# Kernel tuning notes

Measured on AMD Instinct MI355X. Metric: run time of the kernel, lower is better.

Reference implementation:

```python
import jax, jax.numpy as jnp
import numpy as np

QMIN, QMAX = -128.0, 127.0  # symmetric int8 (bit_width=8)

def setup_inputs() -> dict:
    key = jax.random.key(0)
    k1, k2, k3, k4, k5 = jax.random.split(key, 5)
    x = jax.random.normal(k1, (16, 4096, 1024), dtype=jnp.float32)
    weight_int = jax.random.randint(k2, (1024, 1024), 0, 127, dtype=jnp.int32)
    bias_int = jax.random.randint(k3, (1024,), 0, 127, dtype=jnp.int32)
    input_scale = jax.random.uniform(k4, (), dtype=jnp.float32, minval=0.01, maxval=1.0)
    output_scale = jax.random.uniform(k5, (), dtype=jnp.float32, minval=0.01, maxval=1.0)
    return {
        "x": x,
        "weight_int": weight_int,
        "bias_int": bias_int,
        "input_scale": input_scale,
        "output_scale": output_scale,
        "input_zero_point": 0,
        "output_zero_point": 0,
    }

def reference(x, weight_int, bias_int, input_scale, output_scale,
              input_zero_point, output_zero_point):
    # quantize input: round(x/scale)+zp, clamp to int8 range (kept in fp32,
    # matching x_int.float() in the original before the GEMM)
    x_q = jnp.clip(jnp.round(x / input_scale) + input_zero_point, QMIN, QMAX)
    # F.linear(x_q, W, b): [B,S,K] @ [N,K]^T + [N]
    out_int = jnp.einsum('bsk,nk->bsn', x_q, weight_int.astype(jnp.float32))
    out_int = out_int + bias_int.astype(jnp.float32)
    # dequantize output
    return (out_int - output_zero_point) * output_scale
```

## Files before the change

kernel.cpp:

```cpp
#include <hip/hip_runtime.h>
#include <stdint.h>

typedef int v4i __attribute__((ext_vector_type(4)));

#define AS1(p) ((const __attribute__((address_space(1))) void*)(p))
#define AS3(p) ((__attribute__((address_space(3))) void*)(p))

__global__ __launch_bounds__(256) void quant_x_kernel(
    const float* __restrict__ x, int8_t* __restrict__ xq,
    const float* __restrict__ s_p, const int* __restrict__ izp_p, int n16)
{
    int t = blockIdx.x * 256 + threadIdx.x;
    if (t >= n16) return;
    float s = *s_p;
    float zp = (float)(*izp_p);
    const float4* xin = (const float4*)x + (size_t)t * 4;
    int words[4];
#pragma unroll
    for (int i = 0; i < 4; ++i) {
        float4 v = xin[i];
        float q0 = fminf(127.f, fmaxf(-128.f, rintf(v.x / s) + zp));
        float q1 = fminf(127.f, fmaxf(-128.f, rintf(v.y / s) + zp));
        float q2 = fminf(127.f, fmaxf(-128.f, rintf(v.z / s) + zp));
        float q3 = fminf(127.f, fmaxf(-128.f, rintf(v.w / s) + zp));
        words[i] = ((int)q0 & 255) | (((int)q1 & 255) << 8) |
                   (((int)q2 & 255) << 16) | (((int)q3 & 255) << 24);
    }
    ((int4*)xq)[t] = make_int4(words[0], words[1], words[2], words[3]);
}

__global__ __launch_bounds__(256) void pack_w_kernel(
    const int* __restrict__ w, int8_t* __restrict__ w8, int n4)
{
    int t = blockIdx.x * 256 + threadIdx.x;
    if (t >= n4) return;
    int4 v = ((const int4*)w)[t];
    ((int*)w8)[t] = (v.x & 255) | ((v.y & 255) << 8) |
                    ((v.z & 255) << 16) | ((v.w & 255) << 24);
}

#define GM 65536
#define GN 1024
#define GK 1024
#define NT 8

__global__ __launch_bounds__(512, 2) void gemm_i8_kernel(
    const int8_t* __restrict__ A,
    const int8_t* __restrict__ B,
    const int* __restrict__ bias,
    const float* __restrict__ osc_p, const int* __restrict__ ozp_p,
    float* __restrict__ out)
{
    __shared__ int8_t As[2][32768];
    __shared__ int8_t Bs[2][32768];

    const int tid = threadIdx.x;
    const int w   = tid >> 6, l = tid & 63;
    const int wm  = w >> 2,  wn = w & 3;
    const int r15 = l & 15,  s4 = l >> 4;

    const int wg = blockIdx.x;
    const int lg = ((wg & 7) << 7) + (wg >> 3);
    const int bm0 = (lg >> 2) << 8;
    const int bn0 = (lg & 3) << 8;

    const int srow = tid >> 3;
    const int gcol = (((tid & 7) ^ ((tid >> 3) & 7)) << 4);
    const int8_t* aS = A + (size_t)(bm0 + srow) * GK + gcol;
    const int8_t* bS = B + (size_t)(bn0 + srow) * GK + gcol;

#define SHOT_A(T, BUF, C) __builtin_amdgcn_global_load_lds( \
    AS1(aS + (size_t)(C) * 64 * GK + (T) * 128), \
    AS3(&As[BUF][(C) * 8192 + w * 1024]), 16, 0, 0)
#define SHOT_B(T, BUF, C) __builtin_amdgcn_global_load_lds( \
    AS1(bS + (size_t)(C) * 64 * GK + (T) * 128), \
    AS3(&Bs[BUF][(C) * 8192 + w * 1024]), 16, 0, 0)

    const int akey = r15 & 7;
    const int a_rd0 = ((wm * 128 + r15) << 7) + (((0 + s4) ^ akey) << 4);
    const int a_rd1 = ((wm * 128 + r15) << 7) + (((4 + s4) ^ akey) << 4);
    const int b_rd0 = ((wn * 64 + r15) << 7) + (((0 + s4) ^ akey) << 4);
    const int b_rd1 = ((wn * 64 + r15) << 7) + (((4 + s4) ^ akey) << 4);

    v4i acc[8][4];
#pragma unroll
    for (int i = 0; i < 8; ++i)
#pragma unroll
        for (int j = 0; j < 4; ++j) acc[i][j] = (v4i){0, 0, 0, 0};

    v4i bfr[4][2];

#define LOADB(CUR) do { \
    _Pragma("unroll") \
    for (int j = 0; j < 4; ++j) { \
        bfr[j][0] = *(const v4i*)&Bs[CUR][b_rd0 + j * 2048]; \
        bfr[j][1] = *(const v4i*)&Bs[CUR][b_rd1 + j * 2048]; \
    } \
} while (0)

#define PHASE(CUR, Q, ...) do { \
    v4i af0 = *(const v4i*)&As[CUR][a_rd0 + (Q) * 4096]; \
    v4i af1 = *(const v4i*)&As[CUR][a_rd1 + (Q) * 4096]; \
    v4i af2 = *(const v4i*)&As[CUR][a_rd0 + (Q) * 4096 + 2048]; \
    v4i af3 = *(const v4i*)&As[CUR][a_rd1 + (Q) * 4096 + 2048]; \
    __VA_ARGS__; \
    __builtin_amdgcn_s_barrier(); \
    __builtin_amdgcn_s_setprio(1); \
    _Pragma("unroll") \
    for (int j = 0; j < 4; ++j) { \
        acc[(Q)*2][j]     = __builtin_amdgcn_mfma_i32_16x16x64_i8(af0, bfr[j][0], acc[(Q)*2][j], 0, 0, 0); \
        acc[(Q)*2][j]     = __builtin_amdgcn_mfma_i32_16x16x64_i8(af1, bfr[j][1], acc[(Q)*2][j], 0, 0, 0); \
        acc[(Q)*2 + 1][j] = __builtin_amdgcn_mfma_i32_16x16x64_i8(af2, bfr[j][0], acc[(Q)*2 + 1][j], 0, 0, 0); \
        acc[(Q)*2 + 1][j] = __builtin_amdgcn_mfma_i32_16x16x64_i8(af3, bfr[j][1], acc[(Q)*2 + 1][j], 0, 0, 0); \
    } \
    __builtin_amdgcn_s_setprio(0); \
    __builtin_amdgcn_s_barrier(); \
} while (0)

#define BODY(T, SON) do { \
    const int cur_ = (T) & 1, nxt_ = cur_ ^ 1; \
    if (SON) { \
        SHOT_A((T) + 1, nxt_, 0); SHOT_A((T) + 1, nxt_, 1); \
        asm volatile("s_waitcnt vmcnt(2)" ::: "memory"); \
    } else { \
        asm volatile("s_waitcnt vmcnt(0)" ::: "memory"); \
    } \
    __builtin_amdgcn_s_barrier(); \
    __builtin_amdgcn_sched_barrier(0); \
    LOADB(cur_); \
    PHASE(cur_, 0, if (SON) { SHOT_A((T) + 1, nxt_, 2); SHOT_A((T) + 1, nxt_, 3); }); \
    PHASE(cur_, 1, if (SON) { SHOT_B((T) + 1, nxt_, 0); SHOT_B((T) + 1, nxt_, 1); }); \
    PHASE(cur_, 2, if (SON) { SHOT_B((T) + 1, nxt_, 2); SHOT_B((T) + 1, nxt_, 3); }); \
    PHASE(cur_, 3, ); \
} while (0)

#pragma unroll
    for (int c = 0; c < 4; ++c) { SHOT_A(0, 0, c); SHOT_B(0, 0, c); }

#pragma unroll 1
    for (int t = 0; t < NT - 1; ++t) BODY(t, 1);
    BODY(NT - 1, 0);

#undef BODY
#undef PHASE
#undef LOADB
#undef SHOT_A
#undef SHOT_B

    const float osc = *osc_p;
    const int   ozp = *ozp_p;
    int bj[4];
#pragma unroll
    for (int j = 0; j < 4; ++j)
        bj[j] = bias[bn0 + wn * 64 + j * 16 + r15] - ozp;

#pragma unroll
    for (int i = 0; i < 8; ++i) {
        const int mrow = bm0 + wm * 128 + i * 16 + s4 * 4;
#pragma unroll
        for (int j = 0; j < 4; ++j) {
            const int n = bn0 + wn * 64 + j * 16 + r15;
            float* op = out + (size_t)mrow * GN + n;
#pragma unroll
            for (int r = 0; r < 4; ++r)
                __builtin_nontemporal_store((float)(acc[i][j][r] + bj[j]) * osc,
                                            op + (size_t)r * GN);
        }
    }
}

extern "C" void kernel_launch(void* const* d_in, const int* in_sizes, int n_in,
                              void* d_out, int out_size, void* d_ws, size_t ws_size,
                              hipStream_t stream)
{
    const float* x         = (const float*)d_in[0];
    const int*   w_int     = (const int*)d_in[1];
    const int*   b_int     = (const int*)d_in[2];
    const float* in_scale  = (const float*)d_in[3];
    const float* out_scale = (const float*)d_in[4];
    const int*   izp       = (const int*)d_in[5];
    const int*   ozp       = (const int*)d_in[6];
    float* out = (float*)d_out;

    int8_t* xq = (int8_t*)d_ws;
    int8_t* w8 = (int8_t*)d_ws + (size_t)64 * 1024 * 1024;

    quant_x_kernel<<<16384, 256, 0, stream>>>(x, xq, in_scale, izp, 4194304);
    pack_w_kernel<<<1024, 256, 0, stream>>>(w_int, w8, 262144);
    gemm_i8_kernel<<<1024, 512, 0, stream>>>(xq, w8, b_int, out_scale, ozp, out);
}
```

Before: 171.3 us.

## Halve GEMM K-tile to 64 with 16 stages and fuse prep kernels

The int8 GEMM now uses a K-tile of 64 bytes instead of 128, running 16 pipeline iterations. This halves LDS use to 64 KB per block, with a new 4-way XOR swizzle and a restructured load/MFMA phase schedule. The x-quantize and weight-pack kernels are merged into one launch to save a kernel launch. The smaller tile means twice as many barriers per K and less MFMA work per sync, traded for lower LDS footprint and possibly better occupancy.

```diff
diff --git a/kernel.cpp b/kernel.cpp
--- a/kernel.cpp
+++ b/kernel.cpp
@@ -6,12 +6,20 @@
 #define AS1(p) ((const __attribute__((address_space(1))) void*)(p))
 #define AS3(p) ((__attribute__((address_space(3))) void*)(p))
 
-__global__ __launch_bounds__(256) void quant_x_kernel(
+__global__ __launch_bounds__(256) void prep_kernel(
     const float* __restrict__ x, int8_t* __restrict__ xq,
-    const float* __restrict__ s_p, const int* __restrict__ izp_p, int n16)
+    const int* __restrict__ w, int8_t* __restrict__ w8,
+    const float* __restrict__ s_p, const int* __restrict__ izp_p)
 {
-    int t = blockIdx.x * 256 + threadIdx.x;
-    if (t >= n16) return;
+    const int b = blockIdx.x;
+    if (b >= 16384) {
+        int t = (b - 16384) * 256 + threadIdx.x;
+        int4 v = ((const int4*)w)[t];
+        ((int*)w8)[t] = (v.x & 255) | ((v.y & 255) << 8) |
+                        ((v.z & 255) << 16) | ((v.w & 255) << 24);
+        return;
+    }
+    int t = b * 256 + threadIdx.x;
     float s = *s_p;
     float zp = (float)(*izp_p);
     const float4* xin = (const float4*)x + (size_t)t * 4;
@@ -29,20 +37,10 @@
     ((int4*)xq)[t] = make_int4(words[0], words[1], words[2], words[3]);
 }
 
-__global__ __launch_bounds__(256) void pack_w_kernel(
-    const int* __restrict__ w, int8_t* __restrict__ w8, int n4)
-{
-    int t = blockIdx.x * 256 + threadIdx.x;
-    if (t >= n4) return;
-    int4 v = ((const int4*)w)[t];
-    ((int*)w8)[t] = (v.x & 255) | ((v.y & 255) << 8) |
-                    ((v.z & 255) << 16) | ((v.w & 255) << 24);
-}
-
 #define GM 65536
 #define GN 1024
 #define GK 1024
-#define NT 8
+#define NT 16
 
 __global__ __launch_bounds__(512, 2) void gemm_i8_kernel(
     const int8_t* __restrict__ A,
@@ -51,8 +49,8 @@
     const float* __restrict__ osc_p, const int* __restrict__ ozp_p,
     float* __restrict__ out)
 {
-    __shared__ int8_t As[2][32768];
-    __shared__ int8_t Bs[2][32768];
+    __shared__ int8_t As[2][16384];
+    __shared__ int8_t Bs[2][16384];
 
     const int tid = threadIdx.x;
     const int w   = tid >> 6, l = tid & 63;
@@ -64,23 +62,21 @@
     const int bm0 = (lg >> 2) << 8;
     const int bn0 = (lg & 3) << 8;
 
-    const int srow = tid >> 3;
-    const int gcol = (((tid & 7) ^ ((tid >> 3) & 7)) << 4);
+    const int srow = tid >> 2;
+    const int gcol = (((tid & 3) ^ ((tid >> 3) & 3)) << 4);
     const int8_t* aS = A + (size_t)(bm0 + srow) * GK + gcol;
     const int8_t* bS = B + (size_t)(bn0 + srow) * GK + gcol;
 
 #define SHOT_A(T, BUF, C) __builtin_amdgcn_global_load_lds( \
-    AS1(aS + (size_t)(C) * 64 * GK + (T) * 128), \
+    AS1(aS + (size_t)(C) * 128 * GK + (T) * 64), \
     AS3(&As[BUF][(C) * 8192 + w * 1024]), 16, 0, 0)
 #define SHOT_B(T, BUF, C) __builtin_amdgcn_global_load_lds( \
-    AS1(bS + (size_t)(C) * 64 * GK + (T) * 128), \
+    AS1(bS + (size_t)(C) * 128 * GK + (T) * 64), \
     AS3(&Bs[BUF][(C) * 8192 + w * 1024]), 16, 0, 0)
 
-    const int akey = r15 & 7;
-    const int a_rd0 = ((wm * 128 + r15) << 7) + (((0 + s4) ^ akey) << 4);
-    const int a_rd1 = ((wm * 128 + r15) << 7) + (((4 + s4) ^ akey) << 4);
-    const int b_rd0 = ((wn * 64 + r15) << 7) + (((0 + s4) ^ akey) << 4);
-    const int b_rd1 = ((wn * 64 + r15) << 7) + (((4 + s4) ^ akey) << 4);
+    const int key = (r15 >> 1) & 3;
+    const int a_rd = ((wm * 128 + r15) << 6) + ((s4 ^ key) << 4);
+    const int b_rd = ((wn *  64 + r15) << 6) + ((s4 ^ key) << 4);
 
     v4i acc[8][4];
 #pragma unroll
@@ -88,30 +84,19 @@
 #pragma unroll
         for (int j = 0; j < 4; ++j) acc[i][j] = (v4i){0, 0, 0, 0};
 
-    v4i bfr[4][2];
+    v4i bfr[4];
 
-#define LOADB(CUR) do { \
-    _Pragma("unroll") \
-    for (int j = 0; j < 4; ++j) { \
-        bfr[j][0] = *(const v4i*)&Bs[CUR][b_rd0 + j * 2048]; \
-        bfr[j][1] = *(const v4i*)&Bs[CUR][b_rd1 + j * 2048]; \
-    } \
-} while (0)
-
-#define PHASE(CUR, Q, ...) do { \
-    v4i af0 = *(const v4i*)&As[CUR][a_rd0 + (Q) * 4096]; \
-    v4i af1 = *(const v4i*)&As[CUR][a_rd1 + (Q) * 4096]; \
-    v4i af2 = *(const v4i*)&As[CUR][a_rd0 + (Q) * 4096 + 2048]; \
-    v4i af3 = *(const v4i*)&As[CUR][a_rd1 + (Q) * 4096 + 2048]; \
-    __VA_ARGS__; \
+#define PHASE(CUR, P, STMT) do { \
+    v4i af0 = *(const v4i*)&As[CUR][a_rd + (P) * 2048]; \
+    v4i af1 = *(const v4i*)&As[CUR][a_rd + (P) * 2048 + 1024]; \
+    STMT; \
     __builtin_amdgcn_s_barrier(); \
+    asm volatile("s_waitcnt lgkmcnt(0)" ::: "memory"); \
     __builtin_amdgcn_s_setprio(1); \
     _Pragma("unroll") \
     for (int j = 0; j < 4; ++j) { \
-        acc[(Q)*2][j]     = __builtin_amdgcn_mfma_i32_16x16x64_i8(af0, bfr[j][0], acc[(Q)*2][j], 0, 0, 0); \
-        acc[(Q)*2][j]     = __builtin_amdgcn_mfma_i32_16x16x64_i8(af1, bfr[j][1], acc[(Q)*2][j], 0, 0, 0); \
-        acc[(Q)*2 + 1][j] = __builtin_amdgcn_mfma_i32_16x16x64_i8(af2, bfr[j][0], acc[(Q)*2 + 1][j], 0, 0, 0); \
-        acc[(Q)*2 + 1][j] = __builtin_amdgcn_mfma_i32_16x16x64_i8(af3, bfr[j][1], acc[(Q)*2 + 1][j], 0, 0, 0); \
+        acc[(P)*2][j]     = __builtin_amdgcn_mfma_i32_16x16x64_i8(af0, bfr[j], acc[(P)*2][j], 0, 0, 0); \
+        acc[(P)*2 + 1][j] = __builtin_amdgcn_mfma_i32_16x16x64_i8(af1, bfr[j], acc[(P)*2 + 1][j], 0, 0, 0); \
     } \
     __builtin_amdgcn_s_setprio(0); \
     __builtin_amdgcn_s_barrier(); \
@@ -120,22 +105,24 @@
 #define BODY(T, SON) do { \
     const int cur_ = (T) & 1, nxt_ = cur_ ^ 1; \
     if (SON) { \
-        SHOT_A((T) + 1, nxt_, 0); SHOT_A((T) + 1, nxt_, 1); \
-        asm volatile("s_waitcnt vmcnt(2)" ::: "memory"); \
+        SHOT_A((T) + 1, nxt_, 0); \
+        asm volatile("s_waitcnt vmcnt(1)" ::: "memory"); \
     } else { \
         asm volatile("s_waitcnt vmcnt(0)" ::: "memory"); \
     } \
     __builtin_amdgcn_s_barrier(); \
     __builtin_amdgcn_sched_barrier(0); \
-    LOADB(cur_); \
-    PHASE(cur_, 0, if (SON) { SHOT_A((T) + 1, nxt_, 2); SHOT_A((T) + 1, nxt_, 3); }); \
-    PHASE(cur_, 1, if (SON) { SHOT_B((T) + 1, nxt_, 0); SHOT_B((T) + 1, nxt_, 1); }); \
-    PHASE(cur_, 2, if (SON) { SHOT_B((T) + 1, nxt_, 2); SHOT_B((T) + 1, nxt_, 3); }); \
+    PHASE(cur_, 0, { \
+        _Pragma("unroll") \
+        for (int j = 0; j < 4; ++j) bfr[j] = *(const v4i*)&Bs[cur_][b_rd + j * 1024]; \
+        if (SON) SHOT_A((T) + 1, nxt_, 1); }); \
+    PHASE(cur_, 1, { if (SON) SHOT_B((T) + 1, nxt_, 0); }); \
+    PHASE(cur_, 2, { if (SON) SHOT_B((T) + 1, nxt_, 1); }); \
     PHASE(cur_, 3, ); \
 } while (0)
 
-#pragma unroll
-    for (int c = 0; c < 4; ++c) { SHOT_A(0, 0, c); SHOT_B(0, 0, c); }
+    SHOT_A(0, 0, 0); SHOT_A(0, 0, 1);
+    SHOT_B(0, 0, 0); SHOT_B(0, 0, 1);
 
 #pragma unroll 1
     for (int t = 0; t < NT - 1; ++t) BODY(t, 1);
@@ -143,7 +130,6 @@
 
 #undef BODY
 #undef PHASE
-#undef LOADB
 #undef SHOT_A
 #undef SHOT_B
 
@@ -185,7 +171,6 @@
     int8_t* xq = (int8_t*)d_ws;
     int8_t* w8 = (int8_t*)d_ws + (size_t)64 * 1024 * 1024;
 
-    quant_x_kernel<<<16384, 256, 0, stream>>>(x, xq, in_scale, izp, 4194304);
-    pack_w_kernel<<<1024, 256, 0, stream>>>(w_int, w8, 262144);
+    prep_kernel<<<16384 + 1024, 256, 0, stream>>>(x, xq, w_int, w8, in_scale, izp);
     gemm_i8_kernel<<<1024, 512, 0, stream>>>(xq, w8, b_int, out_scale, ozp, out);
 }
```

New measurement: 181.8 us. 1.06x slower.
